# Optimization experiments

Hardware: AMD Instinct MI355X
Metric: run time of the kernel (lower is better)

Reference implementation:

```python
import jax, jax.numpy as jnp
import numpy as np

HIDDEN = 1024
HEADS = 16
HEAD_DIM = HIDDEN // HEADS  # 64
MAX_SEQ = 2048


def _rope_tables():
    # RotaryEmbedding buffers: freqs_cos/sin of shape [max_seq_len, head_dim//2]
    inv_freq = 1.0 / (10000.0 ** (jnp.arange(0, HEAD_DIM, 2, dtype=jnp.float32) / HEAD_DIM))
    t = jnp.arange(MAX_SEQ, dtype=jnp.float32)
    freqs = t[:, None] * inv_freq[None, :]
    return jnp.cos(freqs), jnp.sin(freqs)


def setup_inputs() -> dict:
    key = jax.random.key(0)
    k1, k2, k3 = jax.random.split(key, 3)
    x = jax.random.normal(k1, (2, 2048, HIDDEN), dtype=jnp.float32)
    qkv_w = jax.random.normal(k2, (HIDDEN, 3 * HIDDEN), dtype=jnp.float32) * 0.02
    qkv_b = jnp.zeros((3 * HIDDEN,), dtype=jnp.float32)
    out_w = jax.random.normal(k3, (HIDDEN, HIDDEN), dtype=jnp.float32) * 0.02
    out_b = jnp.zeros((HIDDEN,), dtype=jnp.float32)
    return {"x": x, "qkv_w": qkv_w, "qkv_b": qkv_b, "out_w": out_w, "out_b": out_b}


def reference(x, qkv_w, qkv_b, out_w, out_b):
    b, s, _ = x.shape
    qkv = x @ qkv_w + qkv_b                                   # [b, s, 3*hidden]
    qkv = qkv.reshape(b, s, HEADS, 3 * HEAD_DIM).transpose(0, 2, 1, 3)  # [b, h, s, 3*hd]
    q, k, v = jnp.split(qkv, 3, axis=-1)                      # each [b, h, s, hd]

    # Faithful to source quirk: rotary() is called on [b, h, s, hd] tensors so
    # x.shape[1] == num_heads -> seq_pos = arange(num_heads); tables are indexed
    # by HEAD index and broadcast over the sequence axis.
    cos_tab, sin_tab = _rope_tables()
    cos = cos_tab[:HEADS][None, :, None, :]                   # [1, h, 1, hd/2]
    sin = sin_tab[:HEADS][None, :, None, :]

    def rot(u):
        u1 = u[..., : HEAD_DIM // 2]
        u2 = u[..., HEAD_DIM // 2 :]
        return jnp.concatenate([u1 * cos - u2 * sin, u2 * cos + u1 * sin], axis=-1)

    q = rot(q)
    k = rot(k)

    scores = jnp.einsum("bhqd,bhkd->bhqk", q, k) / (HEAD_DIM ** 0.5)  # [b, h, s, s]
    attn = jax.nn.softmax(scores.astype(jnp.float32), axis=-1).astype(scores.dtype)
    out = jnp.einsum("bhqk,bhkd->bhqd", attn, v)              # [b, h, s, hd]
    out = out.transpose(0, 2, 1, 3).reshape(b, s, HEADS * HEAD_DIM)
    return out @ out_w + out_b
```

## Files before the change

kernel.cpp:

```cpp
#include <hip/hip_runtime.h>
#include <hip/hip_bf16.h>
#include <cstdint>
#include <cstddef>

typedef float  f32x4  __attribute__((ext_vector_type(4)));
typedef __bf16 bf16x8 __attribute__((ext_vector_type(8)));
typedef __bf16 bf16x4 __attribute__((ext_vector_type(4)));

#define HIDDEN 1024
#define SEQ    2048
#define BATCH  2
#define NQKV   3072
#define MTOT   4096

__device__ __forceinline__ __bf16 f2bf(float f) {
  unsigned u = __builtin_bit_cast(unsigned, f);
  u += 0x7FFFu + ((u >> 16) & 1u);
  unsigned short s = (unsigned short)(u >> 16);
  return __builtin_bit_cast(__bf16, s);
}

__device__ __forceinline__ unsigned pk2(float a, float b) {
  unsigned ua = __builtin_bit_cast(unsigned, a) + 0x8000u;
  unsigned ub = __builtin_bit_cast(unsigned, b) + 0x8000u;
  return __builtin_amdgcn_perm(ub, ua, 0x07060302u);
}

__device__ __forceinline__ float fexp2(float x) {
#if __has_builtin(__builtin_amdgcn_exp2f)
  return __builtin_amdgcn_exp2f(x);
#else
  return exp2f(x);
#endif
}

__device__ __forceinline__ void async16(const void* g, void* l) {
  __builtin_amdgcn_global_load_lds((__attribute__((address_space(1))) void*)(g),
                                   (__attribute__((address_space(3))) void*)(l),
                                   16, 0, 0);
}

#define MFMA16(a, b, c) __builtin_amdgcn_mfma_f32_16x16x32_bf16((a), (b), (c), 0, 0, 0)

__global__ __launch_bounds__(256) void k_prep(const float* __restrict__ x,
                                              __bf16* __restrict__ xb,
                                              const float* __restrict__ qkv_w,
                                              __bf16* __restrict__ wqkT,
                                              const float* __restrict__ out_w,
                                              __bf16* __restrict__ woT) {
  __shared__ float tile[64][65];
  const int bid = blockIdx.x, t = threadIdx.x;
  if (bid < 4096) {
    int i = bid * 256 + t;
    float4 v = ((const float4*)x)[i];
    bf16x4 o;
    o[0] = f2bf(v.x); o[1] = f2bf(v.y); o[2] = f2bf(v.z); o[3] = f2bf(v.w);
    ((bf16x4*)xb)[i] = o;
    return;
  }
  const float* W; __bf16* WT; int N, bx, by;
  if (bid < 4864) { int g = bid - 4096; W = qkv_w; WT = wqkT; N = NQKV;  bx = g % 48; by = g / 48; }
  else            { int g = bid - 4864; W = out_w; WT = woT;  N = HIDDEN; bx = g % 16; by = g / 16; }
  const int K = HIDDEN;
  int tx = t & 63, ty = t >> 6;
  int n0 = bx * 64, k0 = by * 64;
#pragma unroll
  for (int r = 0; r < 16; r++) {
    int row = r * 4 + ty;
    tile[row][tx] = W[(size_t)(k0 + row) * N + n0 + tx];
  }
  __syncthreads();
#pragma unroll
  for (int i2 = 0; i2 < 2; i2++) {
    int cc = i2 * 256 + t;
    int n = cc >> 3, ch = cc & 7;
    bf16x8 o;
#pragma unroll
    for (int j = 0; j < 8; j++) o[j] = f2bf(tile[ch * 8 + j][n]);
    *(bf16x8*)(WT + (size_t)(n0 + n) * K + k0 + ch * 8) = o;
  }
}

__global__ __launch_bounds__(512, 2) void k_qkv(const __bf16* __restrict__ A,
                                                const __bf16* __restrict__ BT,
                                                const float* __restrict__ bias,
                                                __bf16* __restrict__ Cout,
                                                __bf16* __restrict__ vt) {
  const int K = HIDDEN;
  __shared__ __align__(16) __bf16 As[2][2][8192];
  __shared__ __align__(16) __bf16 Bs[2][2][8192];
  const int t = threadIdx.x;
  const int lane = t & 63, wv = t >> 6;
  const int ln = lane & 15, quad = lane >> 4;
  const int wm = (wv >> 2) * 128, wn = (wv & 3) * 64;

  const int lin = blockIdx.x;
  const int xcd = lin & 7, wi = lin >> 3;
  const int bxi = (xcd & 3) * 3 + wi % 3;
  const int byi = (xcd >> 2) * 8 + wi / 3;
  const int m0 = byi * 256, n0 = bxi * 256;

  auto stA = [&](int kt, int h) {
    __bf16* dst = &As[kt & 1][h][0];
    const __bf16* src = A + (size_t)m0 * K + kt * 64;
#pragma unroll
    for (int i = 0; i < 2; i++) {
      int tt = i * 512 + t;
      int sr = tt >> 3, ch = tt & 7;
      int gr = (sr & 63) + ((sr >> 6) << 7) + h * 64;
      async16(src + (size_t)gr * K + ((ch ^ (sr & 7)) * 8), dst + tt * 8);
    }
  };
  auto stB = [&](int kt, int h) {
    __bf16* dst = &Bs[kt & 1][h][0];
    const __bf16* src = BT + (size_t)n0 * K + kt * 64;
#pragma unroll
    for (int i = 0; i < 2; i++) {
      int tt = i * 512 + t;
      int sr = tt >> 3, ch = tt & 7;
      int gr = (sr & 63) + ((sr >> 6) << 7) + h * 64;
      async16(src + (size_t)gr * K + ((ch ^ (sr & 7)) * 8), dst + tt * 8);
    }
  };

  const f32x4 zero4 = {0.f, 0.f, 0.f, 0.f};
  f32x4 acc[8][4];
#pragma unroll
  for (int i = 0; i < 8; i++)
#pragma unroll
    for (int j = 0; j < 4; j++) acc[i][j] = zero4;

  stA(0, 0); stA(0, 1); stB(0, 0); stB(0, 1);
  stA(1, 0); stB(1, 0); stB(1, 1);

  bf16x8 af[4][2], bf[4][2];
  const int sra = ln + ((wv >> 2) << 6);
  const int scb = ln + (((wv & 3) >> 1) << 6);
  const int swz = ln & 7;

  const int NT = K / 64;
  for (int kt = 0; kt < NT; kt++) {
    const int p = kt & 1;
    if (kt < NT - 1) asm volatile("s_waitcnt vmcnt(6)" ::: "memory");
    else             asm volatile("s_waitcnt vmcnt(0)" ::: "memory");
    __builtin_amdgcn_s_barrier();
    const __bf16* Bh = &Bs[p][wv & 1][0];
    {
      const __bf16* Ah = &As[p][0][0];
#pragma unroll
      for (int m = 0; m < 4; m++)
#pragma unroll
        for (int kk = 0; kk < 2; kk++)
          af[m][kk] = *(const bf16x8*)(Ah + (sra + m * 16) * 64 + (((kk * 4 + quad) ^ swz) * 8));
#pragma unroll
      for (int n = 0; n < 2; n++)
#pragma unroll
        for (int kk = 0; kk < 2; kk++)
          bf[n][kk] = *(const bf16x8*)(Bh + (scb + n * 16) * 64 + (((kk * 4 + quad) ^ swz) * 8));
      if (kt + 1 < NT) stA(kt + 1, 1);
      __builtin_amdgcn_s_barrier();
      asm volatile("s_waitcnt lgkmcnt(0)" ::: "memory");
      __builtin_amdgcn_sched_barrier(0);
      __builtin_amdgcn_s_setprio(1);
#pragma unroll
      for (int m = 0; m < 4; m++)
#pragma unroll
        for (int n = 0; n < 2; n++) {
          acc[m][n] = MFMA16(af[m][0], bf[n][0], acc[m][n]);
          acc[m][n] = MFMA16(af[m][1], bf[n][1], acc[m][n]);
        }
      __builtin_amdgcn_s_setprio(0);
      __builtin_amdgcn_s_barrier();
    }
    {
#pragma unroll
      for (int n = 2; n < 4; n++)
#pragma unroll
        for (int kk = 0; kk < 2; kk++)
          bf[n][kk] = *(const bf16x8*)(Bh + (scb + n * 16) * 64 + (((kk * 4 + quad) ^ swz) * 8));
      if (kt + 2 < NT) stA(kt + 2, 0);
      __builtin_amdgcn_s_barrier();
      asm volatile("s_waitcnt lgkmcnt(0)" ::: "memory");
      __builtin_amdgcn_sched_barrier(0);
      __builtin_amdgcn_s_setprio(1);
#pragma unroll
      for (int m = 0; m < 4; m++)
#pragma unroll
        for (int n = 2; n < 4; n++) {
          acc[m][n] = MFMA16(af[m][0], bf[n][0], acc[m][n]);
          acc[m][n] = MFMA16(af[m][1], bf[n][1], acc[m][n]);
        }
      __builtin_amdgcn_s_setprio(0);
      __builtin_amdgcn_s_barrier();
    }
    {
      const __bf16* Ah = &As[p][1][0];
#pragma unroll
      for (int m = 0; m < 4; m++)
#pragma unroll
        for (int kk = 0; kk < 2; kk++)
          af[m][kk] = *(const bf16x8*)(Ah + (sra + m * 16) * 64 + (((kk * 4 + quad) ^ swz) * 8));
      if (kt + 2 < NT) stB(kt + 2, 0);
      __builtin_amdgcn_s_barrier();
      asm volatile("s_waitcnt lgkmcnt(0)" ::: "memory");
      __builtin_amdgcn_sched_barrier(0);
      __builtin_amdgcn_s_setprio(1);
#pragma unroll
      for (int m = 0; m < 4; m++)
#pragma unroll
        for (int n = 2; n < 4; n++) {
          acc[4 + m][n] = MFMA16(af[m][0], bf[n][0], acc[4 + m][n]);
          acc[4 + m][n] = MFMA16(af[m][1], bf[n][1], acc[4 + m][n]);
        }
      __builtin_amdgcn_s_setprio(0);
      __builtin_amdgcn_s_barrier();
    }
    {
      if (kt + 2 < NT) stB(kt + 2, 1);
      __builtin_amdgcn_s_setprio(1);
#pragma unroll
      for (int m = 0; m < 4; m++)
#pragma unroll
        for (int n = 0; n < 2; n++) {
          acc[4 + m][n] = MFMA16(af[m][0], bf[n][0], acc[4 + m][n]);
          acc[4 + m][n] = MFMA16(af[m][1], bf[n][1], acc[4 + m][n]);
        }
      __builtin_amdgcn_s_setprio(0);
    }
  }

  const float CE = 0.125f * 1.44269504089f;
#pragma unroll
  for (int nt = 0; nt < 4; nt++) {
    int g = n0 + wn + nt * 16;
    int col = g + ln;
    float bv = bias[col];
    int off = g % 192;
    if (off < 128) {
      float scl = (off < 64) ? CE : 1.0f;
#pragma unroll
      for (int mt = 0; mt < 8; mt++) {
#pragma unroll
        for (int r = 0; r < 4; r++) {
          int row = m0 + wm + mt * 16 + quad * 4 + r;
          Cout[(size_t)row * NQKV + col] = f2bf((acc[mt][nt][r] + bv) * scl);
        }
      }
    } else {
      int hg = g / 192;
      int d  = off - 128 + ln;
#pragma unroll
      for (int mt = 0; mt < 8; mt++) {
        int rowb = m0 + wm + mt * 16;
        int bb = rowb >> 11;
        int s  = rowb & 2047;
        int sblk = s >> 7;
        int blk  = (s >> 4) & 7;
        int pp = (blk & 3) * 32 + quad * 8 + ((blk >> 2) << 2);
        uint2 o;
        o.x = pk2(acc[mt][nt][0] + bv, acc[mt][nt][1] + bv);
        o.y = pk2(acc[mt][nt][2] + bv, acc[mt][nt][3] + bv);
        *(uint2*)(vt + ((size_t)((bb * 16 + hg) * 64 + d)) * SEQ + sblk * 128 + pp) = o;
      }
    }
  }
}

__global__ __launch_bounds__(256, 4) void k_gemm_out(const __bf16* __restrict__ A,
                                                     const __bf16* __restrict__ BT,
                                                     const float* __restrict__ bias,
                                                     float* __restrict__ Cout,
                                                     int M, int N, int K) {
  constexpr int TN = 64;
  __shared__ __align__(16) __bf16 As[2 * 128 * 32];
  __shared__ __align__(16) __bf16 Bs[2 * TN * 32];
  const int t = threadIdx.x;
  const int lane = t & 63, wv = t >> 6;
  const int ln = lane & 15, quad = lane >> 4;
  const int sw8 = (quad ^ ((ln >> 1) & 3)) * 8;
  const int wm = (wv & 1) * 64, wn = (wv >> 1) * (TN / 2);

  const int nbx = N / TN;
  const int cx = nbx >> 1;
  const int lin = blockIdx.x;
  const int xcd = lin & 7, wi = lin >> 3;
  const int bxi = (xcd & 1) * cx + wi % cx;
  const int byi = (xcd >> 1) * 8 + wi / cx;
  const int m0 = byi * 128, n0 = bxi * TN;

  auto stage = [&](int k0, int p) {
    __bf16* Ad = As + p * (128 * 32);
    __bf16* Bd = Bs + p * (TN * 32);
#pragma unroll
    for (int i = 0; i < 2; i++) {
      int tt = i * 256 + t;
      int row = tt >> 2, ch = tt & 3;
      int chs = ch ^ ((row >> 1) & 3);
      async16(A + (size_t)(m0 + row) * K + k0 + chs * 8, Ad + tt * 8);
    }
    {
      int tt = t;
      int row = tt >> 2, ch = tt & 3;
      int chs = ch ^ ((row >> 1) & 3);
      async16(BT + (size_t)(n0 + row) * K + k0 + chs * 8, Bd + tt * 8);
    }
  };

  const f32x4 zero4 = {0.f, 0.f, 0.f, 0.f};
  f32x4 acc[4][2];
#pragma unroll
  for (int i = 0; i < 4; i++)
#pragma unroll
    for (int j = 0; j < 2; j++) acc[i][j] = zero4;

  stage(0, 0);
  const int NIT = K / 32;
  for (int it = 0; it < NIT; it++) {
    __syncthreads();
    if (it + 1 < NIT) stage((it + 1) * 32, (it + 1) & 1);
    const __bf16* Asb = As + (it & 1) * (128 * 32);
    const __bf16* Bsb = Bs + (it & 1) * (TN * 32);
    bf16x8 af[4], bfr[2];
#pragma unroll
    for (int x = 0; x < 4; x++)
      af[x] = *(const bf16x8*)(Asb + (wm + x * 16 + ln) * 32 + sw8);
#pragma unroll
    for (int x = 0; x < 2; x++)
      bfr[x] = *(const bf16x8*)(Bsb + (wn + x * 16 + ln) * 32 + sw8);
#pragma unroll
    for (int mt = 0; mt < 4; mt++)
#pragma unroll
      for (int nt = 0; nt < 2; nt++)
        acc[mt][nt] = MFMA16(af[mt], bfr[nt], acc[mt][nt]);
  }
#pragma unroll
  for (int nt = 0; nt < 2; nt++) {
    int col = n0 + wn + nt * 16 + ln;
    float bv = bias[col];
#pragma unroll
    for (int mt = 0; mt < 4; mt++) {
#pragma unroll
      for (int r = 0; r < 4; r++) {
        int row = m0 + wm + mt * 16 + quad * 4 + r;
        Cout[(size_t)row * N + col] = acc[mt][nt][r] + bv;
      }
    }
  }
}

__global__ __launch_bounds__(512, 4) void k_attn(const __bf16* __restrict__ qkv,
                                                 const __bf16* __restrict__ vt,
                                                 __bf16* __restrict__ aout) {
  __shared__ __align__(16) __bf16 smem[32768];
  const int t = threadIdx.x;
  const int lane = t & 63, wv = t >> 6;
  const int ln = lane & 15, quad = lane >> 4;
  const int sw8 = (quad ^ ((ln >> 1) & 3)) * 8;

  int gid = blockIdx.x;
  int slot = gid & 7, j = gid >> 3;
  int bh = slot * 4 + (j >> 4);
  int qt0 = j & 15;
  const int b = bh >> 4, h = bh & 15;
  const int q0 = qt0 * 128;

  const __bf16* qbase = qkv + (size_t)b * SEQ * NQKV + h * 192;
  const __bf16* kbase = qbase + 64;
  const __bf16* vbase = vt + (size_t)bh * 64 * SEQ;

#pragma unroll
  for (int i = 0; i < 2; i++) {
    int tt = i * 512 + t;
    int hh = tt >> 9, row = (tt >> 2) & 127, ch = tt & 3;
    int chs = ch ^ ((row >> 1) & 3);
    async16(kbase + (size_t)row * NQKV + hh * 32 + chs * 8, smem + tt * 8);
  }
#pragma unroll
  for (int i = 0; i < 2; i++) {
    int tt = i * 512 + t;
    int c = tt >> 8, d = (tt >> 2) & 63, w = tt & 3;
    int ws = w ^ ((d >> 1) & 3);
    async16(vbase + (size_t)d * SEQ + c * 32 + ws * 8, smem + 16384 + tt * 8);
  }

  bf16x8 qf[2];
#pragma unroll
  for (int dc = 0; dc < 2; dc++)
    qf[dc] = *(const bf16x8*)(qbase + (size_t)(q0 + wv * 16 + ln) * NQKV + dc * 32 + quad * 8);

  union { unsigned u[4]; bf16x8 v; } ones;
  ones.u[0] = ones.u[1] = ones.u[2] = ones.u[3] = 0x3F803F80u;

  const f32x4 zero4 = {0.f, 0.f, 0.f, 0.f};
  f32x4 O[4];
  f32x4 Ol = zero4;
#pragma unroll
  for (int dt = 0; dt < 4; dt++) O[dt] = zero4;

  for (int it = 0; it < SEQ / 128; it++) {
    __syncthreads();
    const __bf16* Ks = smem + (it & 1) * 8192;
    const __bf16* Vs = smem + 16384 + (it & 1) * 8192;
    if (it + 1 < SEQ / 128) {
      __bf16* Kd = smem + ((it + 1) & 1) * 8192;
      __bf16* Vd = smem + 16384 + ((it + 1) & 1) * 8192;
      const __bf16* kn = kbase + (size_t)(it + 1) * 128 * NQKV;
      const __bf16* vn = vbase + (it + 1) * 128;
#pragma unroll
      for (int i = 0; i < 2; i++) {
        int tt = i * 512 + t;
        int hh = tt >> 9, row = (tt >> 2) & 127, ch = tt & 3;
        int chs = ch ^ ((row >> 1) & 3);
        async16(kn + (size_t)row * NQKV + hh * 32 + chs * 8, Kd + tt * 8);
      }
#pragma unroll
      for (int i = 0; i < 2; i++) {
        int tt = i * 512 + t;
        int c = tt >> 8, d = (tt >> 2) & 63, w = tt & 3;
        int ws = w ^ ((d >> 1) & 3);
        async16(vn + (size_t)d * SEQ + c * 32 + ws * 8, Vd + tt * 8);
      }
    }

    unsigned Pp[8][2];
#pragma unroll
    for (int blk = 0; blk < 8; blk++) {
      bf16x8 kf0 = *(const bf16x8*)(Ks +        (blk * 16 + ln) * 32 + sw8);
      bf16x8 kf1 = *(const bf16x8*)(Ks + 4096 + (blk * 16 + ln) * 32 + sw8);
      __builtin_amdgcn_s_setprio(1);
      f32x4 s = MFMA16(kf0, qf[0], zero4);
      s = MFMA16(kf1, qf[1], s);
      __builtin_amdgcn_s_setprio(0);
      Pp[blk][0] = pk2(fexp2(s[0]), fexp2(s[1]));
      Pp[blk][1] = pk2(fexp2(s[2]), fexp2(s[3]));
    }
#pragma unroll
    for (int kc = 0; kc < 4; kc++) {
      union { bf16x8 v; unsigned u[4]; } pf;
      pf.u[0] = Pp[kc][0]; pf.u[1] = Pp[kc][1];
      pf.u[2] = Pp[kc + 4][0]; pf.u[3] = Pp[kc + 4][1];
      __builtin_amdgcn_s_setprio(1);
      Ol = MFMA16(pf.v, ones.v, Ol);
#pragma unroll
      for (int dt = 0; dt < 4; dt++) {
        bf16x8 vf = *(const bf16x8*)(Vs + kc * 2048 + (dt * 16 + ln) * 32 + sw8);
        O[dt] = MFMA16(pf.v, vf, O[dt]);
      }
      __builtin_amdgcn_s_setprio(0);
    }
  }

  __bf16* stage = smem + wv * 1024;
#pragma unroll
  for (int r = 0; r < 4; r++) {
    float ir = 1.0f / Ol[r];
#pragma unroll
    for (int dt = 0; dt < 4; dt++)
      stage[(quad * 4 + r) * 64 + dt * 16 + ln] = f2bf(O[dt][r] * ir);
  }
  __bf16* obase = aout + (size_t)(b * SEQ + q0 + wv * 16) * HIDDEN + h * 64;
#pragma unroll
  for (int i = 0; i < 2; i++) {
    int tt = i * 64 + lane; int row = tt >> 3, ch = tt & 7;
    *(bf16x8*)(obase + (size_t)row * HIDDEN + ch * 8) = *(const bf16x8*)(stage + row * 64 + ch * 8);
  }
}

extern "C" void kernel_launch(void* const* d_in, const int* in_sizes, int n_in,
                              void* d_out, int out_size, void* d_ws, size_t ws_size,
                              hipStream_t stream) {
  const float* x     = (const float*)d_in[0];
  const float* qkv_w = (const float*)d_in[1];
  const float* qkv_b = (const float*)d_in[2];
  const float* out_w = (const float*)d_in[3];
  const float* out_b = (const float*)d_in[4];

  char* ws = (char*)d_ws;
  __bf16* xb   = (__bf16*)(ws);
  __bf16* wqkT = (__bf16*)(ws + 8388608);
  __bf16* woT  = (__bf16*)(ws + 14680064);
  __bf16* qkv  = (__bf16*)(ws + 16777216);
  __bf16* vt   = (__bf16*)(ws + 41943040);
  __bf16* aout = (__bf16*)(ws + 50331648);

  k_prep<<<5120, 256, 0, stream>>>(x, xb, qkv_w, wqkT, out_w, woT);
  k_qkv<<<192, 512, 0, stream>>>(xb, wqkT, qkv_b, qkv, vt);
  k_attn<<<512, 512, 0, stream>>>(qkv, vt, aout);
  k_gemm_out<<<512, 256, 0, stream>>>(aout, woT, out_b, (float*)d_out, MTOT, HIDDEN, HIDDEN);
}
```

Baseline: 178.8 us.

## Retile QKV GEMM to 256x192 tiles so grid fills all 256 CUs

```diff
diff --git a/kernel.cpp b/kernel.cpp
--- a/kernel.cpp
+++ b/kernel.cpp
@@ -88,17 +88,17 @@
                                                 __bf16* __restrict__ vt) {
   const int K = HIDDEN;
   __shared__ __align__(16) __bf16 As[2][2][8192];
-  __shared__ __align__(16) __bf16 Bs[2][2][8192];
+  __shared__ __align__(16) __bf16 Bs[2][12288];
   const int t = threadIdx.x;
   const int lane = t & 63, wv = t >> 6;
   const int ln = lane & 15, quad = lane >> 4;
-  const int wm = (wv >> 2) * 128, wn = (wv & 3) * 64;
+  const int wm = (wv >> 2) * 128, wn = (wv & 3) * 48;
 
   const int lin = blockIdx.x;
   const int xcd = lin & 7, wi = lin >> 3;
-  const int bxi = (xcd & 3) * 3 + wi % 3;
-  const int byi = (xcd >> 2) * 8 + wi / 3;
-  const int m0 = byi * 256, n0 = bxi * 256;
+  const int bxi = (xcd & 3) * 4 + (wi & 3);
+  const int byi = (xcd >> 2) * 8 + (wi >> 2);
+  const int m0 = byi * 256, n0 = bxi * 192;
 
   auto stA = [&](int kt, int h) {
     __bf16* dst = &As[kt & 1][h][0];
@@ -111,52 +111,47 @@
       async16(src + (size_t)gr * K + ((ch ^ (sr & 7)) * 8), dst + tt * 8);
     }
   };
-  auto stB = [&](int kt, int h) {
-    __bf16* dst = &Bs[kt & 1][h][0];
+  auto stB = [&](int kt) {
+    __bf16* dst = &Bs[kt & 1][0];
     const __bf16* src = BT + (size_t)n0 * K + kt * 64;
 #pragma unroll
-    for (int i = 0; i < 2; i++) {
+    for (int i = 0; i < 3; i++) {
       int tt = i * 512 + t;
-      int sr = tt >> 3, ch = tt & 7;
-      int gr = (sr & 63) + ((sr >> 6) << 7) + h * 64;
-      async16(src + (size_t)gr * K + ((ch ^ (sr & 7)) * 8), dst + tt * 8);
+      int row = tt >> 3, ch = tt & 7;
+      async16(src + (size_t)row * K + ((ch ^ (row & 7)) * 8), dst + tt * 8);
     }
   };
 
   const f32x4 zero4 = {0.f, 0.f, 0.f, 0.f};
-  f32x4 acc[8][4];
+  f32x4 acc[8][3];
 #pragma unroll
   for (int i = 0; i < 8; i++)
 #pragma unroll
-    for (int j = 0; j < 4; j++) acc[i][j] = zero4;
-
-  stA(0, 0); stA(0, 1); stB(0, 0); stB(0, 1);
-  stA(1, 0); stB(1, 0); stB(1, 1);
-
-  bf16x8 af[4][2], bf[4][2];
+    for (int j = 0; j < 3; j++) acc[i][j] = zero4;
+
+  stA(0, 0); stB(0); stA(0, 1); stA(1, 0); stB(1);
+
+  bf16x8 a0[4], a1[4], b0[3], b1[3];
   const int sra = ln + ((wv >> 2) << 6);
-  const int scb = ln + (((wv & 3) >> 1) << 6);
+  const int srb = (wv & 3) * 48 + ln;
   const int swz = ln & 7;
 
   const int NT = K / 64;
   for (int kt = 0; kt < NT; kt++) {
     const int p = kt & 1;
-    if (kt < NT - 1) asm volatile("s_waitcnt vmcnt(6)" ::: "memory");
+    if (kt < NT - 1) asm volatile("s_waitcnt vmcnt(5)" ::: "memory");
     else             asm volatile("s_waitcnt vmcnt(0)" ::: "memory");
     __builtin_amdgcn_s_barrier();
-    const __bf16* Bh = &Bs[p][wv & 1][0];
+    const __bf16* A0 = &As[p][0][0];
+    const __bf16* A1 = &As[p][1][0];
+    const __bf16* Bb = &Bs[p][0];
     {
-      const __bf16* Ah = &As[p][0][0];
-#pragma unroll
-      for (int m = 0; m < 4; m++)
-#pragma unroll
-        for (int kk = 0; kk < 2; kk++)
-          af[m][kk] = *(const bf16x8*)(Ah + (sra + m * 16) * 64 + (((kk * 4 + quad) ^ swz) * 8));
-#pragma unroll
-      for (int n = 0; n < 2; n++)
-#pragma unroll
-        for (int kk = 0; kk < 2; kk++)
-          bf[n][kk] = *(const bf16x8*)(Bh + (scb + n * 16) * 64 + (((kk * 4 + quad) ^ swz) * 8));
+#pragma unroll
+      for (int m = 0; m < 4; m++)
+        a0[m] = *(const bf16x8*)(A0 + (sra + m * 16) * 64 + ((quad ^ swz) * 8));
+#pragma unroll
+      for (int n = 0; n < 3; n++)
+        b0[n] = *(const bf16x8*)(Bb + (srb + n * 16) * 64 + ((quad ^ swz) * 8));
       if (kt + 1 < NT) stA(kt + 1, 1);
       __builtin_amdgcn_s_barrier();
       asm volatile("s_waitcnt lgkmcnt(0)" ::: "memory");
@@ -165,20 +160,18 @@
 #pragma unroll
       for (int m = 0; m < 4; m++)
 #pragma unroll
-        for (int n = 0; n < 2; n++) {
-          acc[m][n] = MFMA16(af[m][0], bf[n][0], acc[m][n]);
-          acc[m][n] = MFMA16(af[m][1], bf[n][1], acc[m][n]);
-        }
+        for (int n = 0; n < 3; n++)
+          acc[m][n] = MFMA16(a0[m], b0[n], acc[m][n]);
       __builtin_amdgcn_s_setprio(0);
       __builtin_amdgcn_s_barrier();
     }
     {
 #pragma unroll
-      for (int n = 2; n < 4; n++)
-#pragma unroll
-        for (int kk = 0; kk < 2; kk++)
-          bf[n][kk] = *(const bf16x8*)(Bh + (scb + n * 16) * 64 + (((kk * 4 + quad) ^ swz) * 8));
-      if (kt + 2 < NT) stA(kt + 2, 0);
+      for (int m = 0; m < 4; m++)
+        a1[m] = *(const bf16x8*)(A0 + (sra + m * 16) * 64 + (((4 + quad) ^ swz) * 8));
+#pragma unroll
+      for (int n = 0; n < 3; n++)
+        b1[n] = *(const bf16x8*)(Bb + (srb + n * 16) * 64 + (((4 + quad) ^ swz) * 8));
       __builtin_amdgcn_s_barrier();
       asm volatile("s_waitcnt lgkmcnt(0)" ::: "memory");
       __builtin_amdgcn_sched_barrier(0);
@@ -186,21 +179,16 @@
 #pragma unroll
       for (int m = 0; m < 4; m++)
 #pragma unroll
-        for (int n = 2; n < 4; n++) {
-          acc[m][n] = MFMA16(af[m][0], bf[n][0], acc[m][n]);
-          acc[m][n] = MFMA16(af[m][1], bf[n][1], acc[m][n]);
-        }
+        for (int n = 0; n < 3; n++)
+          acc[m][n] = MFMA16(a1[m], b1[n], acc[m][n]);
       __builtin_amdgcn_s_setprio(0);
       __builtin_amdgcn_s_barrier();
     }
     {
-      const __bf16* Ah = &As[p][1][0];
-#pragma unroll
-      for (int m = 0; m < 4; m++)
-#pragma unroll
-        for (int kk = 0; kk < 2; kk++)
-          af[m][kk] = *(const bf16x8*)(Ah + (sra + m * 16) * 64 + (((kk * 4 + quad) ^ swz) * 8));
-      if (kt + 2 < NT) stB(kt + 2, 0);
+#pragma unroll
+      for (int m = 0; m < 4; m++)
+        a0[m] = *(const bf16x8*)(A1 + (sra + m * 16) * 64 + ((quad ^ swz) * 8));
+      if (kt + 2 < NT) stA(kt + 2, 0);
       __builtin_amdgcn_s_barrier();
       asm volatile("s_waitcnt lgkmcnt(0)" ::: "memory");
       __builtin_amdgcn_sched_barrier(0);
@@ -208,30 +196,32 @@
 #pragma unroll
       for (int m = 0; m < 4; m++)
 #pragma unroll
-        for (int n = 2; n < 4; n++) {
-          acc[4 + m][n] = MFMA16(af[m][0], bf[n][0], acc[4 + m][n]);
-          acc[4 + m][n] = MFMA16(af[m][1], bf[n][1], acc[4 + m][n]);
-        }
+        for (int n = 0; n < 3; n++)
+          acc[4 + m][n] = MFMA16(a0[m], b0[n], acc[4 + m][n]);
       __builtin_amdgcn_s_setprio(0);
       __builtin_amdgcn_s_barrier();
     }
     {
-      if (kt + 2 < NT) stB(kt + 2, 1);
-      __builtin_amdgcn_s_setprio(1);
-#pragma unroll
-      for (int m = 0; m < 4; m++)
-#pragma unroll
-        for (int n = 0; n < 2; n++) {
-          acc[4 + m][n] = MFMA16(af[m][0], bf[n][0], acc[4 + m][n]);
-          acc[4 + m][n] = MFMA16(af[m][1], bf[n][1], acc[4 + m][n]);
-        }
+#pragma unroll
+      for (int m = 0; m < 4; m++)
+        a1[m] = *(const bf16x8*)(A1 + (sra + m * 16) * 64 + (((4 + quad) ^ swz) * 8));
+      if (kt + 2 < NT) stB(kt + 2);
+      __builtin_amdgcn_s_barrier();
+      asm volatile("s_waitcnt lgkmcnt(0)" ::: "memory");
+      __builtin_amdgcn_sched_barrier(0);
+      __builtin_amdgcn_s_setprio(1);
+#pragma unroll
+      for (int m = 0; m < 4; m++)
+#pragma unroll
+        for (int n = 0; n < 3; n++)
+          acc[4 + m][n] = MFMA16(a1[m], b1[n], acc[4 + m][n]);
       __builtin_amdgcn_s_setprio(0);
     }
   }
 
   const float CE = 0.125f * 1.44269504089f;
 #pragma unroll
-  for (int nt = 0; nt < 4; nt++) {
+  for (int nt = 0; nt < 3; nt++) {
     int g = n0 + wn + nt * 16;
     int col = g + ln;
     float bv = bias[col];
@@ -484,7 +474,7 @@
   __bf16* aout = (__bf16*)(ws + 50331648);
 
   k_prep<<<5120, 256, 0, stream>>>(x, xb, qkv_w, wqkT, out_w, woT);
-  k_qkv<<<192, 512, 0, stream>>>(xb, wqkT, qkv_b, qkv, vt);
+  k_qkv<<<256, 512, 0, stream>>>(xb, wqkT, qkv_b, qkv, vt);
   k_attn<<<512, 512, 0, stream>>>(qkv, vt, aout);
   k_gemm_out<<<512, 256, 0, stream>>>(aout, woT, out_b, (float*)d_out, MTOT, HIDDEN, HIDDEN);
 }
```

Result: no change. 177.4 us (-0.7%).
